# Kernel tuning notes

Hardware: AMD Instinct MI355X
Metric: run time of the kernel (lower is better)

Reference implementation:

```python
import jax, jax.numpy as jnp
import numpy as np

D, N, F_IN, F_OUT = 2, 4096, 128, 128
DENSITY = 0.005  # avg degree ~20 per row in the 0/1 attention graphs
NEG_INF = -1e30


def setup_inputs() -> dict:
    key = jax.random.key(0)
    ks = jax.random.split(key, 12)
    X = jax.random.normal(ks[0], (D, N, F_IN), dtype=jnp.float32)
    # Dense Laplacian operator used in torch.sparse.mm(L[i], h_p); scaled so tanh stays non-degenerate
    L = jax.random.normal(ks[1], (D, N, N), dtype=jnp.float32) / np.float32(np.sqrt(N))
    # Upper/lower adjacency: 0/1 matrices (GATLayer extracts edges via adj == 1)
    L_u = (jax.random.uniform(ks[2], (D, N, N)) < DENSITY).astype(jnp.float32)
    L_d = (jax.random.uniform(ks[3], (D, N, N)) < DENSITY).astype(jnp.float32)
    s = np.float32(0.05)
    Wp = jax.random.normal(ks[4], (D, F_IN, F_OUT), dtype=jnp.float32) * s
    Ws = jax.random.normal(ks[5], (D, F_IN, F_OUT), dtype=jnp.float32) * s
    Wu = jax.random.normal(ks[6], (D, F_IN, F_OUT), dtype=jnp.float32) * s
    au1 = jax.random.normal(ks[7], (D, F_OUT), dtype=jnp.float32) * s
    au2 = jax.random.normal(ks[8], (D, F_OUT), dtype=jnp.float32) * s
    Wd = jax.random.normal(ks[9], (D, F_IN, F_OUT), dtype=jnp.float32) * s
    ad1 = jax.random.normal(ks[10], (D, F_OUT), dtype=jnp.float32) * s
    ad2 = jax.random.normal(ks[11], (D, F_OUT), dtype=jnp.float32) * s
    return {"X": X, "L": L, "L_u": L_u, "L_d": L_d,
            "Wp": Wp, "Ws": Ws, "Wu": Wu, "au1": au1, "au2": au2,
            "Wd": Wd, "ad1": ad1, "ad2": ad2, "dimensions": D}


def _gat(x, adj, W, a1, a2):
    # GATLayer.forward with boundary=False: linear -> edge scores -> LeakyReLU ->
    # row-wise softmax restricted to adj==1 entries -> sparse mm.
    h = x @ W                                   # [N, F_OUT]
    s1 = h @ a1                                 # [N]  (a_1 linear, bias=False)
    s2 = h @ a2                                 # [N]
    scores = jax.nn.leaky_relu(s1[:, None] + s2[None, :])  # [N, N], slope 0.01
    mask = adj == 1.0
    scores = jnp.where(mask, scores, NEG_INF)
    attn = jax.nn.softmax(scores, axis=1)
    attn = jnp.where(mask, attn, 0.0)           # zero rows with no edges (sparse softmax semantics)
    return attn @ h                             # [N, F_OUT]


def _san_dim(x, L, Lu, Ld, Wp, Ws, Wu, au1, au2, Wd, ad1, ad2):
    h_p = jnp.tanh(L @ (x @ Wp))
    h_s = jnp.tanh(x @ Ws)
    h_u = jnp.tanh(_gat(x, Lu, Wu, au1, au2))
    h_d = jnp.tanh(_gat(x, Ld, Wd, ad1, ad2))
    return h_s + h_u + h_d + h_p


def reference(X, L, L_u, L_d, Wp, Ws, Wu, au1, au2, Wd, ad1, ad2, dimensions):
    # vmap over the `dimensions` simplex levels (all per-level params stacked on axis 0)
    return jax.vmap(_san_dim)(X, L, L_u, L_d, Wp, Ws, Wu, au1, au2, Wd, ad1, ad2)
```

## Files before the change

### kernel.cpp

```cpp
#include <hip/hip_runtime.h>
#include <hip/hip_bf16.h>

#define NN 4096
#define FD 128
#define NDIM 2
#define CAP 256

typedef unsigned long long u64;

#define OFF_HMAT 0
#define OFF_SVEC 3145728
#define OFF_HP   3178496
#define OFF_H0T  7372800
#define OFF_MASK 7897088

typedef _Float16 f16x8 __attribute__((ext_vector_type(8)));
typedef float f32x4 __attribute__((ext_vector_type(4)));
typedef float f32x4v __attribute__((ext_vector_type(4)));
typedef unsigned long long u64x2 __attribute__((ext_vector_type(2)));

union P4 { _Float16 h[4]; int2 i2; };

__device__ __forceinline__ float f4get(const float4& v, int j) {
    return j == 0 ? v.x : j == 1 ? v.y : j == 2 ? v.z : v.w;
}

__global__ __launch_bounds__(256) void k_xw(
    const float* __restrict__ X, const float* __restrict__ Wp,
    const float* __restrict__ Wsm, const float* __restrict__ Wu,
    const float* __restrict__ Wd, const float* __restrict__ au1,
    const float* __restrict__ au2, const float* __restrict__ ad1,
    const float* __restrict__ ad2, float* __restrict__ hmat,
    _Float16* __restrict__ h0T, float* __restrict__ svec) {
  int d = blockIdx.z, p = blockIdx.y;
  int r0 = blockIdx.x * 64;
  const float* W = (p == 0 ? Wp : p == 1 ? Wsm : p == 2 ? Wu : Wd) + (size_t)d * FD * FD;
  const float* Xd = X + ((size_t)d * NN + r0) * FD;
  __shared__ int4 As4[1024];
  __shared__ int4 Bs4[2048];
  char* As = (char*)As4; char* Bs = (char*)Bs4;
  int t = threadIdx.x;

#pragma unroll 4
  for (int u = 0; u < 8; u++) {
    int id = t + u * 256;
    int row = id >> 5, k4 = (id & 31) * 4;
    float4 v = *(const float4*)(Xd + (size_t)row * FD + k4);
    P4 pk;
    pk.h[0] = (_Float16)v.x; pk.h[1] = (_Float16)v.y;
    pk.h[2] = (_Float16)v.z; pk.h[3] = (_Float16)v.w;
    int off = (row * 256 + k4 * 2) ^ ((row & 7) << 4);
    *(int2*)(As + off) = pk.i2;
  }
#pragma unroll 4
  for (int u = 0; u < 16; u++) {
    int id = t + u * 256;
    int k = id >> 5, n4 = (id & 31) * 4;
    float4 v = *(const float4*)(W + (size_t)k * FD + n4);
#pragma unroll
    for (int j = 0; j < 4; j++) {
      int n = n4 + j;
      int off = (n * 256 + k * 2) ^ ((n & 7) << 4);
      *(_Float16*)(Bs + off) = (_Float16)f4get(v, j);
    }
  }
  __syncthreads();

  int w = t >> 6, l = t & 63;
  int lr = l & 15, lkb = (l >> 4) * 16;
  f32x4 acc[8] = {};
#pragma unroll
  for (int kb = 0; kb < 4; kb++) {
    int row = w * 16 + lr;
    int offA = (row * 256 + kb * 64 + lkb) ^ ((row & 7) << 4);
    f16x8 a = *(const f16x8*)(As + offA);
    f16x8 b[8];
#pragma unroll
    for (int n = 0; n < 8; n++) {
      int rn = n * 16 + lr;
      int off = (rn * 256 + kb * 64 + lkb) ^ ((rn & 7) << 4);
      b[n] = *(const f16x8*)(Bs + off);
    }
#pragma unroll
    for (int n = 0; n < 8; n++)
      acc[n] = __builtin_amdgcn_mfma_f32_16x16x32_f16(a, b[n], acc[n], 0, 0, 0);
  }

  if (p == 0) {
    _Float16* hT = h0T + (size_t)d * FD * NN;
#pragma unroll
    for (int n = 0; n < 8; n++) {
      int col = n * 16 + lr;
      int grow = r0 + w * 16 + (l >> 4) * 4;
      P4 pk;
#pragma unroll
      for (int r = 0; r < 4; r++) pk.h[r] = (_Float16)acc[n][r];
      *(int2*)(hT + (size_t)col * NN + grow) = pk.i2;
    }
  } else {
    float* o = hmat + ((size_t)(d * 3 + p - 1) * NN + r0) * FD;
#pragma unroll
    for (int n = 0; n < 8; n++)
#pragma unroll
      for (int r = 0; r < 4; r++)
        o[(size_t)(w * 16 + (l >> 4) * 4 + r) * FD + n * 16 + lr] = acc[n][r];
    if (p >= 2) {
      const float* a1 = (p == 2 ? au1 : ad1) + (size_t)d * FD;
      const float* a2 = (p == 2 ? au2 : ad2) + (size_t)d * FD;
      float av1[8], av2[8];
#pragma unroll
      for (int n = 0; n < 8; n++) {
        av1[n] = a1[n * 16 + lr];
        av2[n] = a2[n * 16 + lr];
      }
      int vb = (d * 4 + (p - 2) * 2);
#pragma unroll
      for (int r = 0; r < 4; r++) {
        float p1 = 0.0f, p2 = 0.0f;
#pragma unroll
        for (int n = 0; n < 8; n++) {
          p1 += acc[n][r] * av1[n];
          p2 += acc[n][r] * av2[n];
        }
#pragma unroll
        for (int o2 = 1; o2 < 16; o2 <<= 1) {
          p1 += __shfl_xor(p1, o2);
          p2 += __shfl_xor(p2, o2);
        }
        if (lr == 0) {
          int row = r0 + w * 16 + (l >> 4) * 4 + r;
          svec[(size_t)vb * NN + row] = p1;
          svec[(size_t)(vb + 1) * NN + row] = p2;
        }
      }
    }
  }
}

__global__ __launch_bounds__(256) void k_mega(
    const float* __restrict__ L, const _Float16* __restrict__ h0T,
    float* __restrict__ hp,
    const float* __restrict__ Lu, const float* __restrict__ Ldn,
    u64* __restrict__ mask) {
  __shared__ int4 sm4[768];
  int t = threadIdx.x, w = t >> 6, lane = t & 63;

  if (blockIdx.x < 512) {
    int b = blockIdx.x;
    int r0 = (b & 63) * 64, ks = (b >> 6) & 3, d = b >> 8;
    const float* Lr = L + (size_t)d * NN * NN;
    const _Float16* hT = h0T + (size_t)d * FD * NN;
    char* As = (char*)sm4;
    char* Bs = (char*)(sm4 + 256);
    int lr = lane & 15, lkb = (lane >> 4) * 16;
    f32x4 acc[8] = {};
    int kbeg = ks * 1024;
    for (int kk = kbeg; kk < kbeg + 1024; kk += 32) {
#pragma unroll
      for (int u = 0; u < 2; u++) {
        int id = t + u * 256;
        int row = id >> 3, k4 = (id & 7) * 4;
        f32x4v v = __builtin_nontemporal_load(
            (const f32x4v*)(Lr + (size_t)(r0 + row) * NN + kk) + (k4 >> 2));
        P4 pk;
        pk.h[0] = (_Float16)v[0]; pk.h[1] = (_Float16)v[1];
        pk.h[2] = (_Float16)v[2]; pk.h[3] = (_Float16)v[3];
        int off = (row * 64 + k4 * 2) ^ ((row & 3) << 4);
        *(int2*)(As + off) = pk.i2;
      }
#pragma unroll
      for (int u = 0; u < 2; u++) {
        int id = t + u * 256;
        int n = id >> 2, k8 = (id & 3) * 8;
        int4 v = *(const int4*)(hT + (size_t)n * NN + kk + k8);
        int off = (n * 64 + k8 * 2) ^ ((n & 3) << 4);
        *(int4*)(Bs + off) = v;
      }
      __syncthreads();
      {
        int row = w * 16 + lr;
        int offA = (row * 64 + lkb) ^ ((row & 3) << 4);
        f16x8 a = *(const f16x8*)(As + offA);
        f16x8 bb[8];
#pragma unroll
        for (int n = 0; n < 8; n++) {
          int rn = n * 16 + lr;
          int off = (rn * 64 + lkb) ^ ((rn & 3) << 4);
          bb[n] = *(const f16x8*)(Bs + off);
        }
#pragma unroll
        for (int n = 0; n < 8; n++)
          acc[n] = __builtin_amdgcn_mfma_f32_16x16x32_f16(a, bb[n], acc[n], 0, 0, 0);
      }
      __syncthreads();
    }
    float* o = hp + ((size_t)(d * 4 + ks) * NN + r0) * FD;
#pragma unroll
    for (int n = 0; n < 8; n++)
#pragma unroll
      for (int r = 0; r < 4; r++)
        o[(size_t)(w * 16 + (lane >> 4) * 4 + r) * FD + n * 16 + lr] = acc[n][r];
    return;
  }

  int hr = (blockIdx.x - 512) * 4 + w;
  int p = hr >> 13;
  int rq = hr & 8191;
  int row = rq >> 1, half = rq & 1;
  const float* src = ((p & 1) ? Ldn : Lu) +
                     ((size_t)(p >> 1) * NN + row) * (size_t)NN + half * 2048;
  f32x4v v[8];
#pragma unroll
  for (int q = 0; q < 4; q++) {
    const f32x4v* s4 = (const f32x4v*)(src + q * 512);
    v[2 * q]     = __builtin_nontemporal_load(s4 + lane);
    v[2 * q + 1] = __builtin_nontemporal_load(s4 + 64 + lane);
  }
  u64* o = mask + ((size_t)p * NN + row) * 64 + half * 32;
#pragma unroll
  for (int q = 0; q < 4; q++) {
    u64 m0 = __ballot(v[2 * q][0] == 1.0f);
    u64 m1 = __ballot(v[2 * q][1] == 1.0f);
    u64 m2 = __ballot(v[2 * q][2] == 1.0f);
    u64 m3 = __ballot(v[2 * q][3] == 1.0f);
    u64 m4 = __ballot(v[2 * q + 1][0] == 1.0f);
    u64 m5 = __ballot(v[2 * q + 1][1] == 1.0f);
    u64 m6 = __ballot(v[2 * q + 1][2] == 1.0f);
    u64 m7 = __ballot(v[2 * q + 1][3] == 1.0f);
    if (lane == 0) {
      u64x2 a0 = {m0, m1}, a1 = {m2, m3}, a2 = {m4, m5}, a3 = {m6, m7};
      __builtin_nontemporal_store(a0, (u64x2*)(o + q * 8 + 0));
      __builtin_nontemporal_store(a1, (u64x2*)(o + q * 8 + 2));
      __builtin_nontemporal_store(a2, (u64x2*)(o + q * 8 + 4));
      __builtin_nontemporal_store(a3, (u64x2*)(o + q * 8 + 6));
    }
  }
}

__global__ __launch_bounds__(256) void k_gatc(
    const u64* __restrict__ mask, const float* __restrict__ hmat,
    const float* __restrict__ svec, const float* __restrict__ hp,
    float* __restrict__ out) {
  int d = blockIdx.y;
  int w = threadIdx.x >> 6, lane = threadIdx.x & 63;
  int i = blockIdx.x * 4 + w;

  __shared__ int ej[4][2][CAP];
  __shared__ float wt[4][2][CAP];

  u64 mm0 = mask[((size_t)((d * 2 + 0) * NN) + i) * 64 + lane];
  u64 mm1 = mask[((size_t)((d * 2 + 1) * NN) + i) * 64 + lane];

  float ga[2][2];
#pragma unroll
  for (int a = 0; a < 2; a++) {
    const float* h = hmat + (size_t)(d * 3 + 1 + a) * NN * FD;
    const float* s1 = svec + (size_t)(d * 4 + 2 * a) * NN;
    const float* s2 = svec + (size_t)(d * 4 + 2 * a + 1) * NN;

    u64 m = a == 0 ? mm0 : mm1;
    int c = __popcll(m);
    int pre = c;
#pragma unroll
    for (int o = 1; o < 64; o <<= 1) {
      int tv = __shfl_up(pre, o);
      if (lane >= o) pre += tv;
    }
    int cnt = __shfl(pre, 63);
    int base = pre - c;
    int colbase = (lane >> 2) * 256 + (lane & 3);
    while (m) {
      int b = __ffsll((unsigned long long)m) - 1;
      m &= m - 1;
      if (base < CAP) ej[w][a][base] = colbase + b * 4;
      base++;
    }
    cnt = min(cnt, CAP);

    float s1i = s1[i];
    float mx = -1e30f;
    for (int e0 = 0; e0 < cnt; e0 += 64) {
      int e = e0 + lane;
      float sc = -1e30f;
      if (e < cnt) {
        int j = ej[w][a][e];
        float x = s1i + s2[j];
        sc = x > 0.0f ? x : 0.01f * x;
        wt[w][a][e] = sc;
      }
      mx = fmaxf(mx, sc);
    }
#pragma unroll
    for (int o = 1; o < 64; o <<= 1) mx = fmaxf(mx, __shfl_xor(mx, o));
    float sum = 0.0f;
    for (int e0 = 0; e0 < cnt; e0 += 64) {
      int e = e0 + lane;
      float pv = 0.0f;
      if (e < cnt) {
        pv = expf(wt[w][a][e] - mx);
        wt[w][a][e] = pv;
      }
      sum += pv;
    }
#pragma unroll
    for (int o = 1; o < 64; o <<= 1) sum += __shfl_xor(sum, o);
    float inv = (cnt > 0) ? 1.0f / sum : 0.0f;

    float acc0 = 0.0f, acc1 = 0.0f;
    int e = 0;
    for (; e + 8 <= cnt; e += 8) {
      const float* rp[8];
      float wg[8];
#pragma unroll
      for (int q = 0; q < 8; q++) {
        rp[q] = h + (size_t)ej[w][a][e + q] * FD;
        wg[q] = wt[w][a][e + q] * inv;
      }
      float va[8], vb[8];
#pragma unroll
      for (int q = 0; q < 8; q++) {
        va[q] = rp[q][lane];
        vb[q] = rp[q][64 + lane];
      }
#pragma unroll
      for (int q = 0; q < 8; q++) {
        acc0 += wg[q] * va[q];
        acc1 += wg[q] * vb[q];
      }
    }
    for (; e + 4 <= cnt; e += 4) {
      const float* r0 = h + (size_t)ej[w][a][e + 0] * FD;
      const float* r1 = h + (size_t)ej[w][a][e + 1] * FD;
      const float* r2 = h + (size_t)ej[w][a][e + 2] * FD;
      const float* r3 = h + (size_t)ej[w][a][e + 3] * FD;
      float w0 = wt[w][a][e + 0] * inv, w1 = wt[w][a][e + 1] * inv;
      float w2 = wt[w][a][e + 2] * inv, w3 = wt[w][a][e + 3] * inv;
      acc0 += w0 * r0[lane] + w1 * r1[lane] + w2 * r2[lane] + w3 * r3[lane];
      acc1 += w0 * r0[64 + lane] + w1 * r1[64 + lane] + w2 * r2[64 + lane] + w3 * r3[64 + lane];
    }
    for (; e < cnt; e++) {
      float wg = wt[w][a][e] * inv;
      const float* hr = h + (size_t)ej[w][a][e] * FD;
      acc0 += wg * hr[lane];
      acc1 += wg * hr[64 + lane];
    }
    ga[a][0] = acc0;
    ga[a][1] = acc1;
  }

  const float* hs = hmat + ((size_t)(d * 3) * NN + i) * FD;
  const float* h0 = hp + ((size_t)(d * 4 + 0) * NN + i) * FD;
  const float* h1 = hp + ((size_t)(d * 4 + 1) * NN + i) * FD;
  const float* h2 = hp + ((size_t)(d * 4 + 2) * NN + i) * FD;
  const float* h3 = hp + ((size_t)(d * 4 + 3) * NN + i) * FD;
  float* o = out + ((size_t)d * NN + i) * FD;
#pragma unroll
  for (int hf = 0; hf < 2; hf++) {
    int col = hf * 64 + lane;
    float ps = h0[col] + h1[col] + h2[col] + h3[col];
    o[col] = tanhf(hs[col]) + tanhf(ga[0][hf]) + tanhf(ga[1][hf]) + tanhf(ps);
  }
}

extern "C" void kernel_launch(void* const* d_in, const int* in_sizes, int n_in,
                              void* d_out, int out_size, void* d_ws, size_t ws_size,
                              hipStream_t stream) {
  const float* X   = (const float*)d_in[0];
  const float* L   = (const float*)d_in[1];
  const float* Lu  = (const float*)d_in[2];
  const float* Ldn = (const float*)d_in[3];
  const float* Wp  = (const float*)d_in[4];
  const float* Wsm = (const float*)d_in[5];
  const float* Wu  = (const float*)d_in[6];
  const float* au1 = (const float*)d_in[7];
  const float* au2 = (const float*)d_in[8];
  const float* Wd  = (const float*)d_in[9];
  const float* ad1 = (const float*)d_in[10];
  const float* ad2 = (const float*)d_in[11];
  float* out = (float*)d_out;
  float* ws = (float*)d_ws;

  float* hmat = ws + OFF_HMAT;
  float* svec = ws + OFF_SVEC;
  float* hp   = ws + OFF_HP;
  _Float16* h0T = (_Float16*)(ws + OFF_H0T);
  u64* mask = (u64*)(ws + OFF_MASK);

  k_xw<<<dim3(NN / 64, 4, NDIM), 256, 0, stream>>>(
      X, Wp, Wsm, Wu, Wd, au1, au2, ad1, ad2, hmat, h0T, svec);
  k_mega<<<dim3(512 + 8192, 1, 1), 256, 0, stream>>>(L, h0T, hp, Lu, Ldn, mask);
  k_gatc<<<dim3(NN / 4, NDIM, 1), 256, 0, stream>>>(mask, hmat, svec, hp, out);
}
```

Before: 130.2 us.

## Regroup stages: fuse XW with mask build, L-GEMM with GAT, add tanh epilogue

Reorganises the three kernels. The XW projection now runs in the same grid as the adjacency mask bitpacking. The dense L·(XWp) GEMM now runs in the same grid as the GAT aggregation. A small third kernel sums the split-K partials, applies tanh and adds the result into the output. The L GEMM tile K-step is also widened from 32 to 64 to halve the barriers per iteration. The aim is to overlap the bandwidth-bound mask reading with compute and to overlap the big GEMM with the gather-heavy GAT work. The cost is an extra launch and an extra read-modify-write pass over the output.

```diff
diff --git a/kernel.cpp b/kernel.cpp
--- a/kernel.cpp
+++ b/kernel.cpp
@@ -25,181 +25,119 @@
     return j == 0 ? v.x : j == 1 ? v.y : j == 2 ? v.z : v.w;
 }
 
-__global__ __launch_bounds__(256) void k_xw(
+__global__ __launch_bounds__(256) void k_a(
     const float* __restrict__ X, const float* __restrict__ Wp,
     const float* __restrict__ Wsm, const float* __restrict__ Wu,
     const float* __restrict__ Wd, const float* __restrict__ au1,
     const float* __restrict__ au2, const float* __restrict__ ad1,
     const float* __restrict__ ad2, float* __restrict__ hmat,
-    _Float16* __restrict__ h0T, float* __restrict__ svec) {
-  int d = blockIdx.z, p = blockIdx.y;
-  int r0 = blockIdx.x * 64;
-  const float* W = (p == 0 ? Wp : p == 1 ? Wsm : p == 2 ? Wu : Wd) + (size_t)d * FD * FD;
-  const float* Xd = X + ((size_t)d * NN + r0) * FD;
-  __shared__ int4 As4[1024];
-  __shared__ int4 Bs4[2048];
-  char* As = (char*)As4; char* Bs = (char*)Bs4;
-  int t = threadIdx.x;
-
-#pragma unroll 4
-  for (int u = 0; u < 8; u++) {
-    int id = t + u * 256;
-    int row = id >> 5, k4 = (id & 31) * 4;
-    float4 v = *(const float4*)(Xd + (size_t)row * FD + k4);
-    P4 pk;
-    pk.h[0] = (_Float16)v.x; pk.h[1] = (_Float16)v.y;
-    pk.h[2] = (_Float16)v.z; pk.h[3] = (_Float16)v.w;
-    int off = (row * 256 + k4 * 2) ^ ((row & 7) << 4);
-    *(int2*)(As + off) = pk.i2;
-  }
-#pragma unroll 4
-  for (int u = 0; u < 16; u++) {
-    int id = t + u * 256;
-    int k = id >> 5, n4 = (id & 31) * 4;
-    float4 v = *(const float4*)(W + (size_t)k * FD + n4);
-#pragma unroll
-    for (int j = 0; j < 4; j++) {
-      int n = n4 + j;
-      int off = (n * 256 + k * 2) ^ ((n & 7) << 4);
-      *(_Float16*)(Bs + off) = (_Float16)f4get(v, j);
-    }
-  }
-  __syncthreads();
-
-  int w = t >> 6, l = t & 63;
-  int lr = l & 15, lkb = (l >> 4) * 16;
-  f32x4 acc[8] = {};
-#pragma unroll
-  for (int kb = 0; kb < 4; kb++) {
-    int row = w * 16 + lr;
-    int offA = (row * 256 + kb * 64 + lkb) ^ ((row & 7) << 4);
-    f16x8 a = *(const f16x8*)(As + offA);
-    f16x8 b[8];
-#pragma unroll
-    for (int n = 0; n < 8; n++) {
-      int rn = n * 16 + lr;
-      int off = (rn * 256 + kb * 64 + lkb) ^ ((rn & 7) << 4);
-      b[n] = *(const f16x8*)(Bs + off);
-    }
-#pragma unroll
-    for (int n = 0; n < 8; n++)
-      acc[n] = __builtin_amdgcn_mfma_f32_16x16x32_f16(a, b[n], acc[n], 0, 0, 0);
-  }
-
-  if (p == 0) {
-    _Float16* hT = h0T + (size_t)d * FD * NN;
-#pragma unroll
-    for (int n = 0; n < 8; n++) {
-      int col = n * 16 + lr;
-      int grow = r0 + w * 16 + (l >> 4) * 4;
-      P4 pk;
-#pragma unroll
-      for (int r = 0; r < 4; r++) pk.h[r] = (_Float16)acc[n][r];
-      *(int2*)(hT + (size_t)col * NN + grow) = pk.i2;
-    }
-  } else {
-    float* o = hmat + ((size_t)(d * 3 + p - 1) * NN + r0) * FD;
-#pragma unroll
-    for (int n = 0; n < 8; n++)
-#pragma unroll
-      for (int r = 0; r < 4; r++)
-        o[(size_t)(w * 16 + (l >> 4) * 4 + r) * FD + n * 16 + lr] = acc[n][r];
-    if (p >= 2) {
-      const float* a1 = (p == 2 ? au1 : ad1) + (size_t)d * FD;
-      const float* a2 = (p == 2 ? au2 : ad2) + (size_t)d * FD;
-      float av1[8], av2[8];
-#pragma unroll
-      for (int n = 0; n < 8; n++) {
-        av1[n] = a1[n * 16 + lr];
-        av2[n] = a2[n * 16 + lr];
-      }
-      int vb = (d * 4 + (p - 2) * 2);
-#pragma unroll
-      for (int r = 0; r < 4; r++) {
-        float p1 = 0.0f, p2 = 0.0f;
-#pragma unroll
-        for (int n = 0; n < 8; n++) {
-          p1 += acc[n][r] * av1[n];
-          p2 += acc[n][r] * av2[n];
-        }
-#pragma unroll
-        for (int o2 = 1; o2 < 16; o2 <<= 1) {
-          p1 += __shfl_xor(p1, o2);
-          p2 += __shfl_xor(p2, o2);
-        }
-        if (lr == 0) {
-          int row = r0 + w * 16 + (l >> 4) * 4 + r;
-          svec[(size_t)vb * NN + row] = p1;
-          svec[(size_t)(vb + 1) * NN + row] = p2;
-        }
-      }
-    }
-  }
-}
-
-__global__ __launch_bounds__(256) void k_mega(
-    const float* __restrict__ L, const _Float16* __restrict__ h0T,
-    float* __restrict__ hp,
+    _Float16* __restrict__ h0T, float* __restrict__ svec,
     const float* __restrict__ Lu, const float* __restrict__ Ldn,
     u64* __restrict__ mask) {
-  __shared__ int4 sm4[768];
+  __shared__ int4 sm4[3072];
   int t = threadIdx.x, w = t >> 6, lane = t & 63;
 
   if (blockIdx.x < 512) {
     int b = blockIdx.x;
-    int r0 = (b & 63) * 64, ks = (b >> 6) & 3, d = b >> 8;
-    const float* Lr = L + (size_t)d * NN * NN;
-    const _Float16* hT = h0T + (size_t)d * FD * NN;
+    int r0 = (b & 63) * 64, p = (b >> 6) & 3, d = b >> 8;
+    const float* W = (p == 0 ? Wp : p == 1 ? Wsm : p == 2 ? Wu : Wd) + (size_t)d * FD * FD;
+    const float* Xd = X + ((size_t)d * NN + r0) * FD;
     char* As = (char*)sm4;
-    char* Bs = (char*)(sm4 + 256);
+    char* Bs = (char*)(sm4 + 1024);
+
+#pragma unroll 4
+    for (int u = 0; u < 8; u++) {
+      int id = t + u * 256;
+      int row = id >> 5, k4 = (id & 31) * 4;
+      float4 v = *(const float4*)(Xd + (size_t)row * FD + k4);
+      P4 pk;
+      pk.h[0] = (_Float16)v.x; pk.h[1] = (_Float16)v.y;
+      pk.h[2] = (_Float16)v.z; pk.h[3] = (_Float16)v.w;
+      int off = (row * 256 + k4 * 2) ^ ((row & 7) << 4);
+      *(int2*)(As + off) = pk.i2;
+    }
+#pragma unroll 4
+    for (int u = 0; u < 16; u++) {
+      int id = t + u * 256;
+      int k = id >> 5, n4 = (id & 31) * 4;
+      float4 v = *(const float4*)(W + (size_t)k * FD + n4);
+#pragma unroll
+      for (int j = 0; j < 4; j++) {
+        int n = n4 + j;
+        int off = (n * 256 + k * 2) ^ ((n & 7) << 4);
+        *(_Float16*)(Bs + off) = (_Float16)f4get(v, j);
+      }
+    }
+    __syncthreads();
+
     int lr = lane & 15, lkb = (lane >> 4) * 16;
     f32x4 acc[8] = {};
-    int kbeg = ks * 1024;
-    for (int kk = kbeg; kk < kbeg + 1024; kk += 32) {
-#pragma unroll
-      for (int u = 0; u < 2; u++) {
-        int id = t + u * 256;
-        int row = id >> 3, k4 = (id & 7) * 4;
-        f32x4v v = __builtin_nontemporal_load(
-            (const f32x4v*)(Lr + (size_t)(r0 + row) * NN + kk) + (k4 >> 2));
+#pragma unroll
+    for (int kb = 0; kb < 4; kb++) {
+      int row = w * 16 + lr;
+      int offA = (row * 256 + kb * 64 + lkb) ^ ((row & 7) << 4);
+      f16x8 a = *(const f16x8*)(As + offA);
+      f16x8 bb[8];
+#pragma unroll
+      for (int n = 0; n < 8; n++) {
+        int rn = n * 16 + lr;
+        int off = (rn * 256 + kb * 64 + lkb) ^ ((rn & 7) << 4);
+        bb[n] = *(const f16x8*)(Bs + off);
+      }
+#pragma unroll
+      for (int n = 0; n < 8; n++)
+        acc[n] = __builtin_amdgcn_mfma_f32_16x16x32_f16(a, bb[n], acc[n], 0, 0, 0);
+    }
+
+    if (p == 0) {
+      _Float16* hT = h0T + (size_t)d * FD * NN;
+#pragma unroll
+      for (int n = 0; n < 8; n++) {
+        int col = n * 16 + lr;
+        int grow = r0 + w * 16 + (lane >> 4) * 4;
         P4 pk;
-        pk.h[0] = (_Float16)v[0]; pk.h[1] = (_Float16)v[1];
-        pk.h[2] = (_Float16)v[2]; pk.h[3] = (_Float16)v[3];
-        int off = (row * 64 + k4 * 2) ^ ((row & 3) << 4);
-        *(int2*)(As + off) = pk.i2;
-      }
-#pragma unroll
-      for (int u = 0; u < 2; u++) {
-        int id = t + u * 256;
-        int n = id >> 2, k8 = (id & 3) * 8;
-        int4 v = *(const int4*)(hT + (size_t)n * NN + kk + k8);
-        int off = (n * 64 + k8 * 2) ^ ((n & 3) << 4);
-        *(int4*)(Bs + off) = v;
-      }
-      __syncthreads();
-      {
-        int row = w * 16 + lr;
-        int offA = (row * 64 + lkb) ^ ((row & 3) << 4);
-        f16x8 a = *(const f16x8*)(As + offA);
-        f16x8 bb[8];
+#pragma unroll
+        for (int r = 0; r < 4; r++) pk.h[r] = (_Float16)acc[n][r];
+        *(int2*)(hT + (size_t)col * NN + grow) = pk.i2;
+      }
+    } else {
+      float* o = hmat + ((size_t)(d * 3 + p - 1) * NN + r0) * FD;
+#pragma unroll
+      for (int n = 0; n < 8; n++)
+#pragma unroll
+        for (int r = 0; r < 4; r++)
+          o[(size_t)(w * 16 + (lane >> 4) * 4 + r) * FD + n * 16 + lr] = acc[n][r];
+      if (p >= 2) {
+        const float* a1 = (p == 2 ? au1 : ad1) + (size_t)d * FD;
+        const float* a2 = (p == 2 ? au2 : ad2) + (size_t)d * FD;
+        float av1[8], av2[8];
 #pragma unroll
         for (int n = 0; n < 8; n++) {
-          int rn = n * 16 + lr;
-          int off = (rn * 64 + lkb) ^ ((rn & 3) << 4);
-          bb[n] = *(const f16x8*)(Bs + off);
+          av1[n] = a1[n * 16 + lr];
+          av2[n] = a2[n * 16 + lr];
         }
-#pragma unroll
-        for (int n = 0; n < 8; n++)
-          acc[n] = __builtin_amdgcn_mfma_f32_16x16x32_f16(a, bb[n], acc[n], 0, 0, 0);
-      }
-      __syncthreads();
-    }
-    float* o = hp + ((size_t)(d * 4 + ks) * NN + r0) * FD;
-#pragma unroll
-    for (int n = 0; n < 8; n++)
-#pragma unroll
-      for (int r = 0; r < 4; r++)
-        o[(size_t)(w * 16 + (lane >> 4) * 4 + r) * FD + n * 16 + lr] = acc[n][r];
+        int vb = (d * 4 + (p - 2) * 2);
+#pragma unroll
+        for (int r = 0; r < 4; r++) {
+          float p1 = 0.0f, p2 = 0.0f;
+#pragma unroll
+          for (int n = 0; n < 8; n++) {
+            p1 += acc[n][r] * av1[n];
+            p2 += acc[n][r] * av2[n];
+          }
+#pragma unroll
+          for (int o2 = 1; o2 < 16; o2 <<= 1) {
+            p1 += __shfl_xor(p1, o2);
+            p2 += __shfl_xor(p2, o2);
+          }
+          if (lr == 0) {
+            int row = r0 + w * 16 + (lane >> 4) * 4 + r;
+            svec[(size_t)vb * NN + row] = p1;
+            svec[(size_t)(vb + 1) * NN + row] = p2;
+          }
+        }
+      }
+    }
     return;
   }
 
@@ -237,16 +175,78 @@
   }
 }
 
-__global__ __launch_bounds__(256) void k_gatc(
-    const u64* __restrict__ mask, const float* __restrict__ hmat,
-    const float* __restrict__ svec, const float* __restrict__ hp,
+__global__ __launch_bounds__(256) void k_b(
+    const float* __restrict__ L, const _Float16* __restrict__ h0T,
+    float* __restrict__ hp, const u64* __restrict__ mask,
+    const float* __restrict__ hmat, const float* __restrict__ svec,
     float* __restrict__ out) {
-  int d = blockIdx.y;
-  int w = threadIdx.x >> 6, lane = threadIdx.x & 63;
-  int i = blockIdx.x * 4 + w;
-
-  __shared__ int ej[4][2][CAP];
-  __shared__ float wt[4][2][CAP];
+  __shared__ int4 sm4[1536];
+  int t = threadIdx.x, w = t >> 6, lane = t & 63;
+
+  if (blockIdx.x < 512) {
+    int b = blockIdx.x;
+    int r0 = (b & 63) * 64, ks = (b >> 6) & 3, d = b >> 8;
+    const float* Lr = L + (size_t)d * NN * NN;
+    const _Float16* hT = h0T + (size_t)d * FD * NN;
+    char* As = (char*)sm4;
+    char* Bs = (char*)(sm4 + 512);
+    int lr = lane & 15, lkb = (lane >> 4) * 16;
+    f32x4 acc[8] = {};
+    int kbeg = ks * 1024;
+    for (int kk = kbeg; kk < kbeg + 1024; kk += 64) {
+#pragma unroll
+      for (int u = 0; u < 4; u++) {
+        int id = t + u * 256;
+        int row = id >> 4, k4 = (id & 15) * 4;
+        f32x4v v = __builtin_nontemporal_load(
+            (const f32x4v*)(Lr + (size_t)(r0 + row) * NN + kk) + (k4 >> 2));
+        P4 pk;
+        pk.h[0] = (_Float16)v[0]; pk.h[1] = (_Float16)v[1];
+        pk.h[2] = (_Float16)v[2]; pk.h[3] = (_Float16)v[3];
+        int off = (row * 128 + k4 * 2) ^ ((row & 7) << 4);
+        *(int2*)(As + off) = pk.i2;
+      }
+#pragma unroll
+      for (int u = 0; u < 4; u++) {
+        int id = t + u * 256;
+        int n = id >> 3, k8 = (id & 7) * 8;
+        int4 v = *(const int4*)(hT + (size_t)n * NN + kk + k8);
+        int off = (n * 128 + k8 * 2) ^ ((n & 7) << 4);
+        *(int4*)(Bs + off) = v;
+      }
+      __syncthreads();
+#pragma unroll
+      for (int kb = 0; kb < 2; kb++) {
+        int row = w * 16 + lr;
+        int offA = (row * 128 + kb * 64 + lkb) ^ ((row & 7) << 4);
+        f16x8 a = *(const f16x8*)(As + offA);
+        f16x8 bb[8];
+#pragma unroll
+        for (int n = 0; n < 8; n++) {
+          int rn = n * 16 + lr;
+          int off = (rn * 128 + kb * 64 + lkb) ^ ((rn & 7) << 4);
+          bb[n] = *(const f16x8*)(Bs + off);
+        }
+#pragma unroll
+        for (int n = 0; n < 8; n++)
+          acc[n] = __builtin_amdgcn_mfma_f32_16x16x32_f16(a, bb[n], acc[n], 0, 0, 0);
+      }
+      __syncthreads();
+    }
+    float* o = hp + ((size_t)(d * 4 + ks) * NN + r0) * FD;
+#pragma unroll
+    for (int n = 0; n < 8; n++)
+#pragma unroll
+      for (int r = 0; r < 4; r++)
+        o[(size_t)(w * 16 + (lane >> 4) * 4 + r) * FD + n * 16 + lr] = acc[n][r];
+    return;
+  }
+
+  int idx = blockIdx.x - 512;
+  int d = idx >> 10;
+  int i = (idx & 1023) * 4 + w;
+  int* ej = (int*)sm4;
+  float* wt = (float*)(sm4 + 512);
 
   u64 mm0 = mask[((size_t)((d * 2 + 0) * NN) + i) * 64 + lane];
   u64 mm1 = mask[((size_t)((d * 2 + 1) * NN) + i) * 64 + lane];
@@ -257,6 +257,8 @@
     const float* h = hmat + (size_t)(d * 3 + 1 + a) * NN * FD;
     const float* s1 = svec + (size_t)(d * 4 + 2 * a) * NN;
     const float* s2 = svec + (size_t)(d * 4 + 2 * a + 1) * NN;
+    int* ejw = ej + (w * 2 + a) * CAP;
+    float* wtw = wt + (w * 2 + a) * CAP;
 
     u64 m = a == 0 ? mm0 : mm1;
     int c = __popcll(m);
@@ -272,7 +274,7 @@
     while (m) {
       int b = __ffsll((unsigned long long)m) - 1;
       m &= m - 1;
-      if (base < CAP) ej[w][a][base] = colbase + b * 4;
+      if (base < CAP) ejw[base] = colbase + b * 4;
       base++;
     }
     cnt = min(cnt, CAP);
@@ -283,10 +285,10 @@
       int e = e0 + lane;
       float sc = -1e30f;
       if (e < cnt) {
-        int j = ej[w][a][e];
+        int j = ejw[e];
         float x = s1i + s2[j];
         sc = x > 0.0f ? x : 0.01f * x;
-        wt[w][a][e] = sc;
+        wtw[e] = sc;
       }
       mx = fmaxf(mx, sc);
     }
@@ -297,8 +299,8 @@
       int e = e0 + lane;
       float pv = 0.0f;
       if (e < cnt) {
-        pv = expf(wt[w][a][e] - mx);
-        wt[w][a][e] = pv;
+        pv = expf(wtw[e] - mx);
+        wtw[e] = pv;
       }
       sum += pv;
     }
@@ -313,8 +315,8 @@
       float wg[8];
 #pragma unroll
       for (int q = 0; q < 8; q++) {
-        rp[q] = h + (size_t)ej[w][a][e + q] * FD;
-        wg[q] = wt[w][a][e + q] * inv;
+        rp[q] = h + (size_t)ejw[e + q] * FD;
+        wg[q] = wtw[e + q] * inv;
       }
       float va[8], vb[8];
 #pragma unroll
@@ -329,18 +331,18 @@
       }
     }
     for (; e + 4 <= cnt; e += 4) {
-      const float* r0 = h + (size_t)ej[w][a][e + 0] * FD;
-      const float* r1 = h + (size_t)ej[w][a][e + 1] * FD;
-      const float* r2 = h + (size_t)ej[w][a][e + 2] * FD;
-      const float* r3 = h + (size_t)ej[w][a][e + 3] * FD;
-      float w0 = wt[w][a][e + 0] * inv, w1 = wt[w][a][e + 1] * inv;
-      float w2 = wt[w][a][e + 2] * inv, w3 = wt[w][a][e + 3] * inv;
+      const float* r0 = h + (size_t)ejw[e + 0] * FD;
+      const float* r1 = h + (size_t)ejw[e + 1] * FD;
+      const float* r2 = h + (size_t)ejw[e + 2] * FD;
+      const float* r3 = h + (size_t)ejw[e + 3] * FD;
+      float w0 = wtw[e + 0] * inv, w1 = wtw[e + 1] * inv;
+      float w2 = wtw[e + 2] * inv, w3 = wtw[e + 3] * inv;
       acc0 += w0 * r0[lane] + w1 * r1[lane] + w2 * r2[lane] + w3 * r3[lane];
       acc1 += w0 * r0[64 + lane] + w1 * r1[64 + lane] + w2 * r2[64 + lane] + w3 * r3[64 + lane];
     }
     for (; e < cnt; e++) {
-      float wg = wt[w][a][e] * inv;
-      const float* hr = h + (size_t)ej[w][a][e] * FD;
+      float wg = wtw[e] * inv;
+      const float* hr = h + (size_t)ejw[e] * FD;
       acc0 += wg * hr[lane];
       acc1 += wg * hr[64 + lane];
     }
@@ -349,16 +351,32 @@
   }
 
   const float* hs = hmat + ((size_t)(d * 3) * NN + i) * FD;
-  const float* h0 = hp + ((size_t)(d * 4 + 0) * NN + i) * FD;
-  const float* h1 = hp + ((size_t)(d * 4 + 1) * NN + i) * FD;
-  const float* h2 = hp + ((size_t)(d * 4 + 2) * NN + i) * FD;
-  const float* h3 = hp + ((size_t)(d * 4 + 3) * NN + i) * FD;
   float* o = out + ((size_t)d * NN + i) * FD;
 #pragma unroll
   for (int hf = 0; hf < 2; hf++) {
     int col = hf * 64 + lane;
-    float ps = h0[col] + h1[col] + h2[col] + h3[col];
-    o[col] = tanhf(hs[col]) + tanhf(ga[0][hf]) + tanhf(ga[1][hf]) + tanhf(ps);
+    o[col] = tanhf(hs[col]) + tanhf(ga[0][hf]) + tanhf(ga[1][hf]);
+  }
+}
+
+__global__ __launch_bounds__(256) void k_ep(
+    const float* __restrict__ hp, float* __restrict__ out) {
+  const size_t tot4 = (size_t)NDIM * NN * FD / 4;
+  for (size_t i4 = (size_t)blockIdx.x * blockDim.x + threadIdx.x; i4 < tot4;
+       i4 += (size_t)gridDim.x * blockDim.x) {
+    size_t i = i4 * 4;
+    int d = (int)(i >> 19);
+    size_t rem = i & 524287;
+    float4 p0 = *(const float4*)(hp + ((size_t)(d * 4 + 0) << 19) + rem);
+    float4 p1 = *(const float4*)(hp + ((size_t)(d * 4 + 1) << 19) + rem);
+    float4 p2 = *(const float4*)(hp + ((size_t)(d * 4 + 2) << 19) + rem);
+    float4 p3 = *(const float4*)(hp + ((size_t)(d * 4 + 3) << 19) + rem);
+    float4 o = *(const float4*)(out + i);
+    o.x += tanhf(p0.x + p1.x + p2.x + p3.x);
+    o.y += tanhf(p0.y + p1.y + p2.y + p3.y);
+    o.z += tanhf(p0.z + p1.z + p2.z + p3.z);
+    o.w += tanhf(p0.w + p1.w + p2.w + p3.w);
+    *(float4*)(out + i) = o;
   }
 }
 
@@ -386,8 +404,9 @@
   _Float16* h0T = (_Float16*)(ws + OFF_H0T);
   u64* mask = (u64*)(ws + OFF_MASK);
 
-  k_xw<<<dim3(NN / 64, 4, NDIM), 256, 0, stream>>>(
-      X, Wp, Wsm, Wu, Wd, au1, au2, ad1, ad2, hmat, h0T, svec);
-  k_mega<<<dim3(512 + 8192, 1, 1), 256, 0, stream>>>(L, h0T, hp, Lu, Ldn, mask);
-  k_gatc<<<dim3(NN / 4, NDIM, 1), 256, 0, stream>>>(mask, hmat, svec, hp, out);
+  k_a<<<dim3(512 + 8192, 1, 1), 256, 0, stream>>>(
+      X, Wp, Wsm, Wu, Wd, au1, au2, ad1, ad2, hmat, h0T, svec, Lu, Ldn, mask);
+  k_b<<<dim3(512 + 2048, 1, 1), 256, 0, stream>>>(
+      L, h0T, hp, mask, hmat, svec, out);
+  k_ep<<<1024, 256, 0, stream>>>(hp, out);
 }
```

Measured after the change: 124.4 us. -4.5%, faster.
